# Kernel optimization log

Hardware: AMD Instinct MI355X
Metric: run time of the kernel (lower is better)

## Reference

```python
import jax, jax.numpy as jnp
import numpy as np

B, T, D, SPAN = 4, 4096, 1024, 128


def _windowed_attention(q, k, v, span):
    # Causal sliding-window attention: position t attends to [max(0, t-span+1), t].
    # Tiled as blocks of size span: each query block attends to its own block
    # plus the previous block (exactly covers the window), avoiding any [T,T]
    # or per-timestep materialization.
    B, T, D = q.shape
    S = span
    nb = T // S  # T chosen divisible by span
    qb = q.reshape(B, nb, S, D)
    kb = k.reshape(B, nb, S, D)
    vb = v.reshape(B, nb, S, D)
    pad = jnp.zeros((B, 1, S, D), dtype=q.dtype)
    kk = jnp.concatenate([jnp.concatenate([pad, kb[:, :-1]], axis=1), kb], axis=2)  # [B,nb,2S,D]
    vv = jnp.concatenate([jnp.concatenate([pad, vb[:, :-1]], axis=1), vb], axis=2)  # [B,nb,2S,D]
    scale = 1.0 / jnp.sqrt(jnp.asarray(D, dtype=q.dtype))
    scores = jnp.einsum('bnqd,bnkd->bnqk', qb, kk) * scale  # [B,nb,S,2S]
    n_idx = jnp.arange(nb)[:, None, None]      # block index
    q_idx = jnp.arange(S)[None, :, None]       # query offset within block
    k_idx = jnp.arange(2 * S)[None, None, :]   # key offset in [prev|cur] pair
    rel = k_idx - S - q_idx                    # key_pos - query_pos
    # window: -span+1 <= rel <= 0; first block's "previous" half is padding -> mask it
    mask = (rel <= 0) & (rel > -S) & ((n_idx > 0) | (k_idx >= S))
    neg = jnp.asarray(jnp.finfo(scores.dtype).min, dtype=scores.dtype)
    scores = jnp.where(mask, scores, neg)
    w = jax.nn.softmax(scores, axis=-1)
    out = jnp.einsum('bnqk,bnkd->bnqd', w, vv)
    return out.reshape(B, T, D)


def setup_inputs() -> dict:
    key = jax.random.key(0)
    ks = jax.random.split(key, 7)
    s = 1.0 / np.sqrt(D)
    return {
        'x': jax.random.normal(ks[0], (B, T, D), dtype=jnp.float32),
        'Wq': jax.random.normal(ks[1], (D, D), dtype=jnp.float32) * s,
        'bq': jax.random.normal(ks[2], (D,), dtype=jnp.float32) * s,
        'Wk': jax.random.normal(ks[3], (D, D), dtype=jnp.float32) * s,
        'bk': jax.random.normal(ks[4], (D,), dtype=jnp.float32) * s,
        'Wv': jax.random.normal(ks[5], (D, D), dtype=jnp.float32) * s,
        'bv': jax.random.normal(ks[6], (D,), dtype=jnp.float32) * s,
        'span': SPAN,
    }


def reference(x, Wq, bq, Wk, bk, Wv, bv, span):
    # torch nn.Linear: y = x @ W.T + b
    q = jnp.einsum('btd,ed->bte', x, Wq) + bq
    k = jnp.einsum('btd,ed->bte', x, Wk) + bk
    v = jnp.einsum('btd,ed->bte', x, Wv) + bv
    return _windowed_attention(q, k, v, span)
```

## Files before the change

kernel.cpp:

```cpp
#include <hip/hip_runtime.h>
#include <hip/hip_bf16.h>

#define BB 4
#define TT 4096
#define DD 1024
#define SS 128
#define NBLK 32
#define MM (BB*TT)

typedef __attribute__((ext_vector_type(8))) short bf16x8;
typedef __attribute__((ext_vector_type(4))) short s16x4;
typedef __attribute__((ext_vector_type(4))) float f32x4;

__device__ __forceinline__ short f2bf(float f) {
    union { float f; unsigned u; } cv; cv.f = f;
    unsigned u = cv.u;
    u += 0x7fffu + ((u >> 16) & 1u);
    return (short)(u >> 16);
}

__device__ __forceinline__ void gload16(const short* g, short* l) {
    __builtin_amdgcn_global_load_lds(
        (const __attribute__((address_space(1))) void*)g,
        (__attribute__((address_space(3))) void*)l, 16, 0, 0);
}

__global__ __launch_bounds__(256) void cast_f32_bf16(
    const float* __restrict__ src, short* __restrict__ dst)
{
    const int i = (blockIdx.x * 256 + threadIdx.x) * 4;
    const float4 v = *(const float4*)(src + i);
    s16x4 o;
    o.x = f2bf(v.x); o.y = f2bf(v.y); o.z = f2bf(v.z); o.w = f2bf(v.w);
    *(s16x4*)(dst + i) = o;
}

__global__ __launch_bounds__(256) void cast_w3(
    const float* __restrict__ a, const float* __restrict__ b,
    const float* __restrict__ c, short* __restrict__ dst)
{
    const float* src = (blockIdx.y == 0) ? a : (blockIdx.y == 1) ? b : c;
    short* d = dst + (size_t)blockIdx.y * DD * DD;
    const int i = (blockIdx.x * 256 + threadIdx.x) * 4;
    const float4 v = *(const float4*)(src + i);
    s16x4 o;
    o.x = f2bf(v.x); o.y = f2bf(v.y); o.z = f2bf(v.z); o.w = f2bf(v.w);
    *(s16x4*)(d + i) = o;
}

__global__ __launch_bounds__(256) void qkv_gemm(
    const short* __restrict__ X,
    const short* __restrict__ W3,
    const float* __restrict__ bq, const float* __restrict__ bk,
    const float* __restrict__ bv,
    short* __restrict__ q, short* __restrict__ k, short* __restrict__ vT)
{
    __shared__ short As[128 * 32];
    __shared__ short Bs[128 * 32];

    const int tid = threadIdx.x;
    const int l   = blockIdx.x;
    const int xcd = l & 7;
    const int rr  = l >> 3;
    const int m0  = (xcd * 16 + (rr & 15)) * 128;
    const int n_idx = rr >> 4;
    const int grp = n_idx >> 3;
    const int n0g = (n_idx & 7) * 128;

    const short* W = W3 + (size_t)grp * DD * DD;
    const float* bias = (grp == 0) ? bq : (grp == 1) ? bk : bv;

    const int wv   = tid >> 6, lane = tid & 63;
    const int wm   = wv >> 1,  wn   = wv & 1;
    const int quad = lane >> 4, c16 = lane & 15;
    const int srow = lane >> 2;
    const int scol = (lane & 3) * 8;

    f32x4 acc[4][4];
#pragma unroll
    for (int i = 0; i < 4; i++)
#pragma unroll
        for (int j = 0; j < 4; j++) acc[i][j] = (f32x4){0.f, 0.f, 0.f, 0.f};

    if (grp != 2) {
        for (int k0 = 0; k0 < DD; k0 += 32) {
            __syncthreads();
#pragma unroll
            for (int s = 0; s < 2; s++) {
                const int row = (wv * 2 + s) * 16 + srow;
                gload16(X + (m0 + row) * DD + k0 + scol, As + row * 32 + scol);
                gload16(W + (n0g + row) * DD + k0 + scol, Bs + row * 32 + scol);
            }
            __syncthreads();
            bf16x8 af[4], bfr[4];
#pragma unroll
            for (int i = 0; i < 4; i++)
                af[i] = *(const bf16x8*)(As + (wm * 64 + i * 16 + c16) * 32 + quad * 8);
#pragma unroll
            for (int j = 0; j < 4; j++)
                bfr[j] = *(const bf16x8*)(Bs + (wn * 64 + j * 16 + c16) * 32 + quad * 8);
#pragma unroll
            for (int i = 0; i < 4; i++)
#pragma unroll
                for (int j = 0; j < 4; j++)
                    acc[i][j] = __builtin_amdgcn_mfma_f32_16x16x32_bf16(af[i], bfr[j], acc[i][j], 0, 0, 0);
        }
        short* Y = (grp == 0) ? q : k;
#pragma unroll
        for (int j = 0; j < 4; j++) {
            const int col = n0g + wn * 64 + j * 16 + c16;
            const float bc = bias[col];
#pragma unroll
            for (int i = 0; i < 4; i++) {
                const int row = m0 + wm * 64 + i * 16 + quad * 4;
#pragma unroll
                for (int r = 0; r < 4; r++)
                    Y[(row + r) * DD + col] = f2bf(acc[i][j][r] + bc);
            }
        }
    } else {
        for (int k0 = 0; k0 < DD; k0 += 32) {
            __syncthreads();
#pragma unroll
            for (int s = 0; s < 2; s++) {
                const int row = (wv * 2 + s) * 16 + srow;
                gload16(X + (m0 + row) * DD + k0 + scol, As + row * 32 + scol);
                gload16(W + (n0g + row) * DD + k0 + scol, Bs + row * 32 + scol);
            }
            __syncthreads();
            bf16x8 af[4], bfr[4];
#pragma unroll
            for (int i = 0; i < 4; i++)
                af[i] = *(const bf16x8*)(As + (wm * 64 + i * 16 + c16) * 32 + quad * 8);
#pragma unroll
            for (int j = 0; j < 4; j++)
                bfr[j] = *(const bf16x8*)(Bs + (wn * 64 + j * 16 + c16) * 32 + quad * 8);
#pragma unroll
            for (int i = 0; i < 4; i++)
#pragma unroll
                for (int j = 0; j < 4; j++)
                    acc[i][j] = __builtin_amdgcn_mfma_f32_16x16x32_bf16(bfr[j], af[i], acc[i][j], 0, 0, 0);
        }
        const int b  = m0 >> 12;
        const int t0 = m0 & 4095;
#pragma unroll
        for (int j = 0; j < 4; j++) {
#pragma unroll
            for (int r = 0; r < 4; r++) {
                const int drow = n0g + wn * 64 + j * 16 + quad * 4 + r;
                const float bc = bias[drow];
#pragma unroll
                for (int i = 0; i < 4; i++) {
                    const int tcol = t0 + wm * 64 + i * 16 + c16;
                    vT[(b * DD + drow) * TT + tcol] = f2bf(acc[i][j][r] + bc);
                }
            }
        }
    }
}

__global__ __launch_bounds__(256) void attn_fused(
    const short* __restrict__ Q,
    const short* __restrict__ Kb,
    const short* __restrict__ VT,
    float* __restrict__ O)
{
    __shared__ short lds[57856];

    const int l   = blockIdx.x;
    const int xcd = l & 7;
    const int rr  = l >> 3;
    const int n   = xcd * 4 + (rr & 3);
    const int qh  = (rr >> 2) & 1;
    const int b   = rr >> 3;

    const int tid  = threadIdx.x;
    const int wv   = tid >> 6, lane = tid & 63;
    const int quad = lane >> 4, c16 = lane & 15;
    const int srow = tid >> 2;
    const int scol = (tid & 3) * 8;

    const int qrow   = b * TT + n * SS + qh * 64;
    const int krow   = b * TT + n * SS - SS;
    const int bstart = b * TT;

    f32x4 acc[16];
#pragma unroll
    for (int j = 0; j < 16; j++) acc[j] = (f32x4){0.f, 0.f, 0.f, 0.f};

    auto stage1 = [&](int kk, short* qb, short* kbuf) {
        const int k0 = kk * 64;
#pragma unroll
        for (int ks = 0; ks < 2; ks++) {
            gload16(Q + (qrow + srow) * DD + k0 + ks * 32 + scol,
                    qb + ks * 2048 + srow * 32 + scol);
#pragma unroll
            for (int s = 0; s < 4; s++) {
                const int row = srow + s * 64;
                int g = krow + row;
                if (g < bstart) g = bstart;
                gload16(Kb + g * DD + k0 + ks * 32 + scol,
                        kbuf + ks * 8192 + row * 32 + scol);
            }
        }
    };

    stage1(0, lds, lds + 4096);
    for (int kk = 0; kk < 16; kk++) {
        __syncthreads();
        if (kk < 15) {
            const int o = ((kk + 1) & 1) * 20480;
            stage1(kk + 1, lds + o, lds + o + 4096);
        }
        const int cb = (kk & 1) * 20480;
        const short* qb = lds + cb;
        const short* kbuf = lds + cb + 4096;
#pragma unroll
        for (int ks = 0; ks < 2; ks++) {
            bf16x8 a = *(const bf16x8*)(qb + ks * 2048 + (wv * 16 + c16) * 32 + quad * 8);
#pragma unroll
            for (int j = 0; j < 16; j++) {
                bf16x8 bf = *(const bf16x8*)(kbuf + ks * 8192 + (j * 16 + c16) * 32 + quad * 8);
                acc[j] = __builtin_amdgcn_mfma_f32_16x16x32_bf16(a, bf, acc[j], 0, 0, 0);
            }
        }
    }

    short* Pw = lds + 40960 + wv * (16 * 264);
    const float scale = 0.03125f;
#pragma unroll
    for (int r = 0; r < 4; r++) {
        const int q_idx = qh * 64 + wv * 16 + quad * 4 + r;
        float mx = -3.0e38f;
#pragma unroll
        for (int j = 0; j < 16; j++) {
            const int k_idx = j * 16 + c16;
            const int rel = k_idx - SS - q_idx;
            const bool valid = (rel <= 0) & (rel > -SS) & ((n > 0) | (k_idx >= SS));
            const float sv = valid ? acc[j][r] * scale : -3.0e38f;
            acc[j][r] = sv;
            mx = fmaxf(mx, sv);
        }
#pragma unroll
        for (int o = 1; o < 16; o <<= 1) mx = fmaxf(mx, __shfl_xor(mx, o));
        float sm = 0.f;
#pragma unroll
        for (int j = 0; j < 16; j++) {
            const float p = __expf(acc[j][r] - mx);
            acc[j][r] = p;
            sm += p;
        }
#pragma unroll
        for (int o = 1; o < 16; o <<= 1) sm += __shfl_xor(sm, o);
        const float inv = 1.0f / sm;
#pragma unroll
        for (int j = 0; j < 16; j++)
            Pw[(quad * 4 + r) * 264 + j * 16 + c16] = f2bf(acc[j][r] * inv);
    }

    const int tbase = n * SS - SS;
    auto stage2 = [&](int s, short* vbuf) {
        const int d0 = (s >> 1) * 128;
        const int kh = (s & 1) * 128;
#pragma unroll
        for (int kc = 0; kc < 4; kc++) {
#pragma unroll
            for (int s64 = 0; s64 < 2; s64++) {
                const int row = srow + s64 * 64;
                int t = tbase + kh + kc * 32 + scol;
                if (t < 0) t = 0;
                gload16(VT + (size_t)(b * DD + d0 + row) * TT + t,
                        vbuf + kc * 4096 + row * 32 + scol);
            }
        }
    };

    __syncthreads();
    stage2(0, lds);
    f32x4 o8[8];
#pragma unroll
    for (int j = 0; j < 8; j++) o8[j] = (f32x4){0.f, 0.f, 0.f, 0.f};

    for (int s = 0; s < 16; s++) {
        __syncthreads();
        if (s < 15) stage2(s + 1, lds + ((s + 1) & 1) * 16384);
        const short* vbuf = lds + (s & 1) * 16384;
        const int kh = (s & 1) * 128;
#pragma unroll
        for (int kc = 0; kc < 4; kc++) {
            bf16x8 a = *(const bf16x8*)(Pw + c16 * 264 + kh + kc * 32 + quad * 8);
#pragma unroll
            for (int jj = 0; jj < 8; jj++) {
                bf16x8 bf = *(const bf16x8*)(vbuf + kc * 4096 + (jj * 16 + c16) * 32 + quad * 8);
                o8[jj] = __builtin_amdgcn_mfma_f32_16x16x32_bf16(a, bf, o8[jj], 0, 0, 0);
            }
        }
        if (s & 1) {
            const int d0 = (s >> 1) * 128;
#pragma unroll
            for (int jj = 0; jj < 8; jj++) {
#pragma unroll
                for (int r = 0; r < 4; r++)
                    O[(size_t)(qrow + wv * 16 + quad * 4 + r) * DD + d0 + jj * 16 + c16] = o8[jj][r];
                o8[jj] = (f32x4){0.f, 0.f, 0.f, 0.f};
            }
        }
    }
}

extern "C" void kernel_launch(void* const* d_in, const int* in_sizes, int n_in,
                              void* d_out, int out_size, void* d_ws, size_t ws_size,
                              hipStream_t stream) {
    const float* x  = (const float*)d_in[0];
    const float* Wq = (const float*)d_in[1];
    const float* bq = (const float*)d_in[2];
    const float* Wk = (const float*)d_in[3];
    const float* bk = (const float*)d_in[4];
    const float* Wv = (const float*)d_in[5];
    const float* bv = (const float*)d_in[6];
    float* out = (float*)d_out;

    char* ws = (char*)d_ws;
    const size_t SZ = (size_t)MM * DD * 2;
    short* q   = (short*)(ws);
    short* k   = (short*)(ws + SZ);
    short* vT  = (short*)(ws + 2 * SZ);
    short* xb  = (short*)(ws + 3 * SZ);
    short* w3b = (short*)(ws + 4 * SZ);

    dim3 blk(256);
    cast_f32_bf16<<<MM * DD / 1024, blk, 0, stream>>>(x, xb);
    cast_w3<<<dim3(DD * DD / 1024, 3), blk, 0, stream>>>(Wq, Wk, Wv, w3b);

    qkv_gemm<<<3072, blk, 0, stream>>>(xb, w3b, bq, bk, bv, q, k, vT);

    attn_fused<<<256, blk, 0, stream>>>(q, k, vT, out);
}
```

Baseline: 320.7 us.

## Multi-buffer GEMM and attention loads with explicit vmcnt waits

The QKV GEMM now double-buffers its LDS tiles, issuing the next k-slice's global-to-LDS loads before computing the current one, which also drops one barrier per iteration. The attention kernel moves from two-stage to three-stage buffering in both the QK and PV loops. It replaces full __syncthreads with precise s_waitcnt vmcnt counts plus a bare barrier, and prefetches the first V tiles before the softmax. This aims to hide global load latency behind MFMA work, at the cost of more LDS (about 153 KB per attention block). The hand-tuned vmcnt counts also depend on the exact number and order of outstanding loads and stores.

```diff
diff --git a/kernel.cpp b/kernel.cpp
--- a/kernel.cpp
+++ b/kernel.cpp
@@ -11,6 +11,14 @@
 typedef __attribute__((ext_vector_type(8))) short bf16x8;
 typedef __attribute__((ext_vector_type(4))) short s16x4;
 typedef __attribute__((ext_vector_type(4))) float f32x4;
+
+#define VMCNT(N) asm volatile("s_waitcnt vmcnt(" #N ")" ::: "memory")
+
+__device__ __forceinline__ void block_sync() {
+    asm volatile("" ::: "memory");
+    __builtin_amdgcn_s_barrier();
+    asm volatile("" ::: "memory");
+}
 
 __device__ __forceinline__ short f2bf(float f) {
     union { float f; unsigned u; } cv; cv.f = f;
@@ -55,8 +63,8 @@
     const float* __restrict__ bv,
     short* __restrict__ q, short* __restrict__ k, short* __restrict__ vT)
 {
-    __shared__ short As[128 * 32];
-    __shared__ short Bs[128 * 32];
+    __shared__ short As[2][4096];
+    __shared__ short Bs[2][4096];
 
     const int tid = threadIdx.x;
     const int l   = blockIdx.x;
@@ -76,29 +84,39 @@
     const int srow = lane >> 2;
     const int scol = (lane & 3) * 8;
 
+    auto stage = [&](int kk) {
+        short* as = As[kk & 1];
+        short* bs = Bs[kk & 1];
+        const int k0 = kk * 32;
+#pragma unroll
+        for (int s = 0; s < 2; s++) {
+            const int row = (wv * 2 + s) * 16 + srow;
+            gload16(X + (m0 + row) * DD + k0 + scol, as + row * 32 + scol);
+            gload16(W + (n0g + row) * DD + k0 + scol, bs + row * 32 + scol);
+        }
+    };
+
     f32x4 acc[4][4];
 #pragma unroll
     for (int i = 0; i < 4; i++)
 #pragma unroll
         for (int j = 0; j < 4; j++) acc[i][j] = (f32x4){0.f, 0.f, 0.f, 0.f};
 
+    stage(0);
+
     if (grp != 2) {
-        for (int k0 = 0; k0 < DD; k0 += 32) {
+        for (int kk = 0; kk < 32; kk++) {
             __syncthreads();
-#pragma unroll
-            for (int s = 0; s < 2; s++) {
-                const int row = (wv * 2 + s) * 16 + srow;
-                gload16(X + (m0 + row) * DD + k0 + scol, As + row * 32 + scol);
-                gload16(W + (n0g + row) * DD + k0 + scol, Bs + row * 32 + scol);
-            }
-            __syncthreads();
+            if (kk < 31) stage(kk + 1);
+            const short* as = As[kk & 1];
+            const short* bs = Bs[kk & 1];
             bf16x8 af[4], bfr[4];
 #pragma unroll
             for (int i = 0; i < 4; i++)
-                af[i] = *(const bf16x8*)(As + (wm * 64 + i * 16 + c16) * 32 + quad * 8);
+                af[i] = *(const bf16x8*)(as + (wm * 64 + i * 16 + c16) * 32 + quad * 8);
 #pragma unroll
             for (int j = 0; j < 4; j++)
-                bfr[j] = *(const bf16x8*)(Bs + (wn * 64 + j * 16 + c16) * 32 + quad * 8);
+                bfr[j] = *(const bf16x8*)(bs + (wn * 64 + j * 16 + c16) * 32 + quad * 8);
 #pragma unroll
             for (int i = 0; i < 4; i++)
 #pragma unroll
@@ -119,22 +137,18 @@
             }
         }
     } else {
-        for (int k0 = 0; k0 < DD; k0 += 32) {
+        for (int kk = 0; kk < 32; kk++) {
             __syncthreads();
-#pragma unroll
-            for (int s = 0; s < 2; s++) {
-                const int row = (wv * 2 + s) * 16 + srow;
-                gload16(X + (m0 + row) * DD + k0 + scol, As + row * 32 + scol);
-                gload16(W + (n0g + row) * DD + k0 + scol, Bs + row * 32 + scol);
-            }
-            __syncthreads();
+            if (kk < 31) stage(kk + 1);
+            const short* as = As[kk & 1];
+            const short* bs = Bs[kk & 1];
             bf16x8 af[4], bfr[4];
 #pragma unroll
             for (int i = 0; i < 4; i++)
-                af[i] = *(const bf16x8*)(As + (wm * 64 + i * 16 + c16) * 32 + quad * 8);
+                af[i] = *(const bf16x8*)(as + (wm * 64 + i * 16 + c16) * 32 + quad * 8);
 #pragma unroll
             for (int j = 0; j < 4; j++)
-                bfr[j] = *(const bf16x8*)(Bs + (wn * 64 + j * 16 + c16) * 32 + quad * 8);
+                bfr[j] = *(const bf16x8*)(bs + (wn * 64 + j * 16 + c16) * 32 + quad * 8);
 #pragma unroll
             for (int i = 0; i < 4; i++)
 #pragma unroll
@@ -165,7 +179,7 @@
     const short* __restrict__ VT,
     float* __restrict__ O)
 {
-    __shared__ short lds[57856];
+    __shared__ short lds[78336];
 
     const int l   = blockIdx.x;
     const int xcd = l & 7;
@@ -188,7 +202,9 @@
 #pragma unroll
     for (int j = 0; j < 16; j++) acc[j] = (f32x4){0.f, 0.f, 0.f, 0.f};
 
-    auto stage1 = [&](int kk, short* qb, short* kbuf) {
+    auto stage1 = [&](int kk, int bi) {
+        short* qb   = lds + bi * 20480;
+        short* kbuf = qb + 4096;
         const int k0 = kk * 64;
 #pragma unroll
         for (int ks = 0; ks < 2; ks++) {
@@ -205,16 +221,14 @@
         }
     };
 
-    stage1(0, lds, lds + 4096);
+    stage1(0, 0);
+    stage1(1, 1);
     for (int kk = 0; kk < 16; kk++) {
-        __syncthreads();
-        if (kk < 15) {
-            const int o = ((kk + 1) & 1) * 20480;
-            stage1(kk + 1, lds + o, lds + o + 4096);
-        }
-        const int cb = (kk & 1) * 20480;
-        const short* qb = lds + cb;
-        const short* kbuf = lds + cb + 4096;
+        if (kk < 15) { VMCNT(10); } else { VMCNT(0); }
+        block_sync();
+        if (kk < 14) stage1(kk + 2, (kk + 2) % 3);
+        const short* qb   = lds + (kk % 3) * 20480;
+        const short* kbuf = qb + 4096;
 #pragma unroll
         for (int ks = 0; ks < 2; ks++) {
             bf16x8 a = *(const bf16x8*)(qb + ks * 2048 + (wv * 16 + c16) * 32 + quad * 8);
@@ -226,7 +240,28 @@
         }
     }
 
-    short* Pw = lds + 40960 + wv * (16 * 264);
+    __syncthreads();
+
+    const int tbase = n * SS - SS;
+    auto stage2 = [&](int s, short* vbuf) {
+        const int d0 = (s >> 1) * 128;
+        const int kh = (s & 1) * 128;
+#pragma unroll
+        for (int kc = 0; kc < 4; kc++) {
+#pragma unroll
+            for (int s64 = 0; s64 < 2; s64++) {
+                const int row = srow + s64 * 64;
+                int t = tbase + kh + kc * 32 + scol;
+                if (t < 0) t = 0;
+                gload16(VT + (size_t)(b * DD + d0 + row) * TT + t,
+                        vbuf + kc * 4096 + row * 32 + scol);
+            }
+        }
+    };
+    stage2(0, lds);
+    stage2(1, lds + 16384);
+
+    short* Pw = lds + 61440 + wv * (16 * 264);
     const float scale = 0.03125f;
 #pragma unroll
     for (int r = 0; r < 4; r++) {
@@ -258,33 +293,17 @@
             Pw[(quad * 4 + r) * 264 + j * 16 + c16] = f2bf(acc[j][r] * inv);
     }
 
-    const int tbase = n * SS - SS;
-    auto stage2 = [&](int s, short* vbuf) {
-        const int d0 = (s >> 1) * 128;
-        const int kh = (s & 1) * 128;
-#pragma unroll
-        for (int kc = 0; kc < 4; kc++) {
-#pragma unroll
-            for (int s64 = 0; s64 < 2; s64++) {
-                const int row = srow + s64 * 64;
-                int t = tbase + kh + kc * 32 + scol;
-                if (t < 0) t = 0;
-                gload16(VT + (size_t)(b * DD + d0 + row) * TT + t,
-                        vbuf + kc * 4096 + row * 32 + scol);
-            }
-        }
-    };
-
-    __syncthreads();
-    stage2(0, lds);
     f32x4 o8[8];
 #pragma unroll
     for (int j = 0; j < 8; j++) o8[j] = (f32x4){0.f, 0.f, 0.f, 0.f};
 
     for (int s = 0; s < 16; s++) {
-        __syncthreads();
-        if (s < 15) stage2(s + 1, lds + ((s + 1) & 1) * 16384);
-        const short* vbuf = lds + (s & 1) * 16384;
+        if (s < 2)       { VMCNT(8); }
+        else if (s < 15) { VMCNT(40); }
+        else             { VMCNT(0); }
+        block_sync();
+        if (s < 14) stage2(s + 2, lds + ((s + 2) % 3) * 16384);
+        const short* vbuf = lds + (s % 3) * 16384;
         const int kh = (s & 1) * 128;
 #pragma unroll
         for (int kc = 0; kc < 4; kc++) {
```

After: 320.9 us. Within noise of the previous version (+0.0%).
